# Performance work log

Measured on AMD Instinct MI355X. Metric: run time of the kernel, lower is better.

The kernel has to match this reference:

```python
import jax, jax.numpy as jnp
import numpy as np

PI = 3.1415927410125732
N = 4096
VELOCITY = 5e-7
RC = 3.15e-6          # collision radius
RR = 8e-6             # repulsion radius
RO = 2.5e-5           # orientation radius (Ra = inf -> inside_Ra all-true)
ALPHA = PI            # field of view; < 2*pi so within_view masking is active
DT_TRANS = 1.4e-14    # translational diffusion DT
DR = 0.0028
GAMMA = 25.0
DT = 0.2              # timestep dt
COLLISION_ITERS = 3   # fixed-iteration version of recursive solve_collisions
EPS = 1e-14


def _c(x):  # [N,2] real -> complex64
    return jax.lax.complex(x[..., 0], x[..., 1])


def _r(z):  # complex -> [..., 2] real
    return jnp.stack([z.real, z.imag], axis=-1)


def _anglediff(a, b):
    # torch get_anglediff: wrap angle(a)-angle(b) into (-pi, pi)
    diff = jnp.angle(a) - jnp.angle(b)
    diff = jnp.where(diff <= -PI, jnp.mod(diff, PI), diff)
    return diff - (diff >= PI) * (2.0 * PI)


def _cossim(a, b):
    # nn.CosineSimilarity(dim=1, eps=1e-14) on view_as_real of complex vectors
    dot = a.real * b.real + a.imag * b.imag
    na = jnp.sqrt(a.real ** 2 + a.imag ** 2 + 1e-30)
    nb = jnp.sqrt(b.real ** 2 + b.imag ** 2 + 1e-30)
    return dot / (jnp.maximum(na, EPS) * jnp.maximum(nb, EPS))


def setup_inputs() -> dict:
    key = jax.random.key(0)
    k1, k2, k3, k4, k5 = jax.random.split(key, 5)
    positions = jax.random.normal(k1, (N, 2), jnp.float32) * 5e-4
    ang = jax.random.uniform(k2, (N,), jnp.float32, -PI, PI)
    orientations = jnp.stack([jnp.cos(ang), jnp.sin(ang)], axis=-1)  # unit complex
    Deltas = jax.random.uniform(k3, (1,), jnp.float32, 0.1, 0.6)
    rot_noise = jax.random.normal(k4, (N,), jnp.float32)
    trans_noise = jax.random.normal(k5, (N, 2), jnp.float32)
    return {"positions": positions, "orientations": orientations, "Deltas": Deltas,
            "rot_noise": rot_noise, "trans_noise": trans_noise}


def reference(positions, orientations, Deltas, rot_noise, trans_noise):
    p = _c(positions)      # [N] complex positions
    u = _c(orientations)   # [N] complex orientations
    n = p.shape[0]
    eye = jnp.eye(n, dtype=bool)

    # pairwise direction/distance: dirs[i,j] = p_j - p_i
    dirs = p[None, :] - p[:, None]
    dists = jnp.abs(dirs)

    inside_Rr = (dists <= RR) & ~eye
    inside_Ro = dists <= RO + RC
    # inside_Ra with Ra = inf is all-True

    # angle between separation vector and orientation of the *neighbor* j
    ang_diff = _anglediff(dirs, u[None, :])
    in_front = ang_diff < PI / 2
    within_view = ang_diff < ALPHA  # alpha < 2*pi branch active

    cdtype = p.dtype
    mask_rr = (inside_Rr & in_front).astype(cdtype)
    mask_ra = within_view.astype(cdtype)  # inside_Ra all True
    mask_ro = (inside_Ro & within_view).astype(cdtype)

    n_r = mask_rr.real.sum(axis=1)
    S = (mask_rr @ p) / jnp.maximum(n_r, 1.0) - p * jnp.sign(n_r)
    d = -S

    n_a = mask_ra.real.sum(axis=1)
    cms = (mask_ra @ p) / jnp.maximum(n_a, 1.0)
    Ps = cms - p * jnp.sign(n_a)

    orientation_sums = mask_ro @ u

    leftturns = Ps * jnp.exp(1j * Deltas)
    rightturns = Ps * jnp.exp(-1j * Deltas)

    # T >= T_release branch: pick the turn most aligned with neighbor orientations
    left_closer = _cossim(leftturns, orientation_sums) >= _cossim(rightturns, orientation_sums)
    best_turns = jnp.where(left_closer, leftturns, rightturns)

    d_abs = jnp.abs(d)
    d_safe = jnp.where(d_abs > 0, d, jnp.ones((), cdtype))
    best_safe = jnp.where(jnp.abs(best_turns) > 0, best_turns, jnp.ones((), cdtype))
    angle_to_target = jnp.where(d_abs > 0, _anglediff(d_safe, u), _anglediff(best_safe, u))

    # rotational_noise = randn * sqrt(2*DR); rotation = exp(i*(dt*Gamma*DR*sin + noise*sqrt(dt)))
    rot = jnp.exp(1j * (DT * GAMMA * DR * jnp.sin(angle_to_target)
                        + rot_noise * np.float32(np.sqrt(2 * DR)) * np.float32(np.sqrt(DT))))

    # complex-normal translational noise (per-component std 1/sqrt(2)) * sqrt(2*DT) * sqrt(dt)
    tn = _c(trans_noise) * np.float32(np.sqrt(0.5)) * np.float32(np.sqrt(2 * DT_TRANS))
    translation = DT * VELOCITY * u + tn * np.float32(np.sqrt(DT))

    def collide(i, pos):
        dd = pos[None, :] - pos[:, None]
        dd_nd = jnp.where(eye, jnp.ones((), pos.dtype), dd)  # avoid 0/0 on diagonal
        ab = jnp.where(eye, 0.0, jnp.abs(dd_nd))
        coll = ab <= 2 * RC - jnp.eye(n, dtype=ab.dtype)
        safe = jnp.where(coll, ab, 1.0)
        move = jnp.where(coll, dd / safe * ((2.1 * RC - ab) * 0.5), jnp.zeros((), pos.dtype))
        return pos - move.sum(axis=1)

    new_p = jax.lax.fori_loop(0, COLLISION_ITERS, collide, p + translation)
    new_u = u * rot

    # pack the 5 complex outputs as real [5, N, 2]
    return jnp.stack([_r(new_p), _r(new_u), _r(orientation_sums), _r(leftturns), _r(rightturns)], axis=0)
```

## Files before the change

kernel.cpp:

```cpp
#include <hip/hip_runtime.h>
#include <math.h>

#define NPART 4096
#define NBLK  1024
#define NTHR  256
#define IPB   4
#define SMAX  256
#define PPT   (NPART / NTHR)

constexpr float RORC   = (float)(2.5e-5 + 3.15e-6);
constexpr float RORC2  = RORC * RORC;
constexpr float RRF    = 8e-6f;
constexpr float RR2    = RRF * RRF;
constexpr float TWORC  = (float)(2.0 * 3.15e-6);
constexpr float TWORC2 = TWORC * TWORC;
constexpr float C21RC  = (float)(2.1 * 3.15e-6);
constexpr float RCAND2 = 1.6e-9f;
constexpr float C_ROT  = (float)(0.2 * 25.0 * 0.0028);
constexpr float C_RN1  = (float)0.07483314773547883;
constexpr float C_SQDT = (float)0.4472135954999579;
constexpr float C_TRV  = (float)(0.2 * 5e-7);
constexpr float C_HALF = (float)0.7071067811865476;
constexpr float C_SQ2T = (float)1.6733200530681511e-07;
constexpr float EPSF   = 1e-14f;

__global__ __launch_bounds__(NTHR, 4) void fused_all(
        const float2* __restrict__ pos, const float2* __restrict__ ori,
        const float* __restrict__ Deltas, const float* __restrict__ rot_noise,
        const float2* __restrict__ trans_noise, float2* __restrict__ out) {
    __shared__ float    sred[2 * NTHR];
    __shared__ float    res[5][IPB];
    __shared__ unsigned bmap[NPART / 32];
    __shared__ int      Sidx[SMAX];
    __shared__ float4   posS4[SMAX / 2];
    __shared__ int      scnt;
    float2* posS = (float2*)posS4;
    const float4* __restrict__ pos4 = (const float4*)pos;

    const int tid  = threadIdx.x;
    const int il   = tid >> 6;
    const int lane = tid & 63;
    const int base = blockIdx.x * IPB;
    const int gi   = base + il;

    const float2 pi   = pos[gi];
    const float  delv = Deltas[0];
    float rn_early = 0.f;
    if (tid < IPB) rn_early = rot_noise[base + tid];
    {
        const float2 ow = ori[tid * 16];
        const float2 tw = trans_noise[tid * 16];
        asm volatile("" :: "v"(ow.x), "v"(ow.y), "v"(tw.x), "v"(tw.y));
    }

    if (tid == 0) scnt = IPB;
    if (tid < IPB) Sidx[tid] = base + tid;
    if (tid < NPART / 32) {
        const int seedw = base >> 5;
        bmap[tid] = (tid == seedw) ? (0xFu << (base & 31)) : 0u;
    }

    float mx = 0.f, my = 0.f;
    #pragma unroll
    for (int k = 0; k < PPT; ++k) {
        const float2 v = pos[k * NTHR + tid];
        mx += v.x; my += v.y;
    }
    sred[tid] = mx; sred[NTHR + tid] = my;
    __syncthreads();

    float nr = 0.f, sx = 0.f, sy = 0.f, oxs = 0.f, oys = 0.f;
    #pragma unroll 2
    for (int t = lane; t < NPART / 2; t += 64) {
        const float4 w = pos4[t];
        const float dx0 = w.x - pi.x, dy0 = w.y - pi.y;
        const float r20 = fmaf(dx0, dx0, dy0 * dy0);
        const float dx1 = w.z - pi.x, dy1 = w.w - pi.y;
        const float r21 = fmaf(dx1, dx1, dy1 * dy1);
        if (fminf(r20, r21) > RCAND2) continue;
        if (r20 <= RCAND2) {
            const int j = 2 * t;
            const unsigned bit = 1u << (j & 31);
            const unsigned old = atomicOr(&bmap[j >> 5], bit);
            if (!(old & bit)) {
                const int slot = atomicAdd(&scnt, 1);
                if (slot < SMAX) Sidx[slot] = j;
            }
            if (r20 <= RORC2) {
                const float2 uj = ori[j];
                oxs += uj.x; oys += uj.y;
                if (r20 <= RR2 && r20 > 0.f) {
                    const float dt_ = fmaf(dx0, uj.x, dy0 * uj.y);
                    const float cr_ = fmaf(dy0, uj.x, -dx0 * uj.y);
                    if (!((dt_ <= 0.f) && (cr_ >= 0.f))) {
                        nr += 1.f; sx += w.x; sy += w.y;
                    }
                }
            }
        }
        if (r21 <= RCAND2) {
            const int j = 2 * t + 1;
            const unsigned bit = 1u << (j & 31);
            const unsigned old = atomicOr(&bmap[j >> 5], bit);
            if (!(old & bit)) {
                const int slot = atomicAdd(&scnt, 1);
                if (slot < SMAX) Sidx[slot] = j;
            }
            if (r21 <= RORC2) {
                const float2 uj = ori[j];
                oxs += uj.x; oys += uj.y;
                if (r21 <= RR2 && r21 > 0.f) {
                    const float dt_ = fmaf(dx1, uj.x, dy1 * uj.y);
                    const float cr_ = fmaf(dy1, uj.x, -dx1 * uj.y);
                    if (!((dt_ <= 0.f) && (cr_ >= 0.f))) {
                        nr += 1.f; sx += w.z; sy += w.w;
                    }
                }
            }
        }
    }
    {
        float vals[5] = {nr, sx, sy, oxs, oys};
        #pragma unroll
        for (int q = 0; q < 5; ++q)
            #pragma unroll
            for (int off = 32; off >= 1; off >>= 1)
                vals[q] += __shfl_down(vals[q], off);
        if (lane == 0) {
            res[0][il] = vals[0]; res[1][il] = vals[1]; res[2][il] = vals[2];
            res[3][il] = vals[3]; res[4][il] = vals[4];
        }
    }
    __syncthreads();

    const int nS = (scnt < SMAX) ? scnt : SMAX;
    if (tid < 128) {
        sred[tid]        += sred[tid + 128];
        sred[NTHR + tid] += sred[NTHR + tid + 128];
    }
    if (tid < nS) {
        const int p = Sidx[tid];
        const float2 pq = pos[p];
        const float2 uu = ori[p];
        const float2 tn = trans_noise[p];
        posS[tid] = make_float2(
            pq.x + (C_TRV * uu.x + ((tn.x * C_HALF) * C_SQ2T) * C_SQDT),
            pq.y + (C_TRV * uu.y + ((tn.y * C_HALF) * C_SQ2T) * C_SQDT));
    }
    __syncthreads();

    if (tid < 64) {
        sred[tid]        += sred[tid + 64];
        sred[NTHR + tid] += sred[NTHR + tid + 64];
    }
    __syncthreads();

    float cmx = 0.f, cmy = 0.f;
    if (il == 0) {
        float vx = sred[lane];
        float vy = sred[NTHR + lane];
        #pragma unroll
        for (int off = 32; off >= 1; off >>= 1) {
            vx += __shfl_down(vx, off);
            vy += __shfl_down(vy, off);
        }
        cmx = __shfl(vx, 0) * (1.f / NPART);
        cmy = __shfl(vy, 0) * (1.f / NPART);
    }

    if (tid < IPB) {
        const int g2 = base + tid;
        const float2 p = pos[g2];
        const float2 u = ori[g2];
        const float nrv = res[0][tid], sxv = res[1][tid], syv = res[2][tid];
        const float osx = res[3][tid], osy = res[4][tid];

        const float inv = 1.f / fmaxf(nrv, 1.f);
        const float sg  = (nrv > 0.f) ? 1.f : 0.f;
        const float Sx = sxv * inv - p.x * sg;
        const float Sy = syv * inv - p.y * sg;
        const float dxv = -Sx, dyv = -Sy;

        const float Psx = cmx - p.x;
        const float Psy = cmy - p.y;

        float sd, cd;
        sincosf(delv, &sd, &cd);
        const float Lx = Psx * cd - Psy * sd;
        const float Ly = Psx * sd + Psy * cd;
        const float Rx = Psx * cd + Psy * sd;
        const float Ry = Psy * cd - Psx * sd;

        const float no  = fmaxf(sqrtf(osx * osx + osy * osy + 1e-30f), EPSF);
        const float nl  = fmaxf(sqrtf(Lx * Lx + Ly * Ly + 1e-30f), EPSF);
        const float nrr = fmaxf(sqrtf(Rx * Rx + Ry * Ry + 1e-30f), EPSF);
        const float csl = (Lx * osx + Ly * osy) / (nl * no);
        const float csr = (Rx * osx + Ry * osy) / (nrr * no);
        const bool left = (csl >= csr);
        const float bx = left ? Lx : Rx;
        const float by = left ? Ly : Ry;

        float cx, cy;
        if (dxv != 0.f || dyv != 0.f)    { cx = dxv; cy = dyv; }
        else if (bx != 0.f || by != 0.f) { cx = bx;  cy = by;  }
        else                             { cx = 1.f; cy = 0.f; }

        const float dt_ = cx * u.x + cy * u.y;
        const float cr_ = cy * u.x - cx * u.y;
        const float sin_t = cr_ / sqrtf(dt_ * dt_ + cr_ * cr_);

        const float ang = C_ROT * sin_t + (rn_early * C_RN1) * C_SQDT;
        float sa, ca;
        sincosf(ang, &sa, &ca);
        out[1 * NPART + g2] = make_float2(u.x * ca - u.y * sa,
                                          u.x * sa + u.y * ca);
        out[2 * NPART + g2] = make_float2(osx, osy);
        out[3 * NPART + g2] = make_float2(Lx, Ly);
        out[4 * NPART + g2] = make_float2(Rx, Ry);
    }

    for (int pass = 0; pass < 3; ++pass) {
        float px = 1e9f, py = 1e9f, ax = 0.f, ay = 0.f;
        const bool mv = (tid < nS);
        if (mv) { px = posS[tid].x; py = posS[tid].y; }
        int b = 0;
        for (; b + 4 <= nS; b += 4) {
            const float4 w0 = posS4[(b >> 1)];
            const float4 w1 = posS4[(b >> 1) + 1];
            const float bxs[4] = {w0.x, w0.z, w1.x, w1.z};
            const float bys[4] = {w0.y, w0.w, w1.y, w1.w};
            #pragma unroll
            for (int s = 0; s < 4; ++s) {
                const float dx = bxs[s] - px, dy = bys[s] - py;
                const float r2 = fmaf(dx, dx, dy * dy);
                if (r2 <= TWORC2 && r2 > 0.f) {
                    const float ab = sqrtf(r2);
                    const float sc = (C21RC - ab) * 0.5f / ab;
                    ax = fmaf(dx, sc, ax);
                    ay = fmaf(dy, sc, ay);
                }
            }
        }
        for (; b < nS; ++b) {
            const float2 pb = posS[b];
            const float dx = pb.x - px, dy = pb.y - py;
            const float r2 = fmaf(dx, dx, dy * dy);
            if (r2 <= TWORC2 && r2 > 0.f) {
                const float ab = sqrtf(r2);
                const float sc = (C21RC - ab) * 0.5f / ab;
                ax = fmaf(dx, sc, ax);
                ay = fmaf(dy, sc, ay);
            }
        }
        __syncthreads();
        if (mv) posS[tid] = make_float2(px - ax, py - ay);
        __syncthreads();
    }
    if (tid < IPB)
        out[0 * NPART + base + tid] = posS[tid];
}

extern "C" void kernel_launch(void* const* d_in, const int* in_sizes, int n_in,
                              void* d_out, int out_size, void* d_ws, size_t ws_size,
                              hipStream_t stream) {
    const float2* pos = (const float2*)d_in[0];
    const float2* ori = (const float2*)d_in[1];
    const float*  del = (const float*)d_in[2];
    const float*  rn  = (const float*)d_in[3];
    const float2* tn  = (const float2*)d_in[4];
    float2* o2 = (float2*)d_out;
    (void)d_ws; (void)ws_size;

    fused_all<<<dim3(NBLK), dim3(NTHR), 0, stream>>>(pos, ori, del, rn, tn, o2);
}
```

Before: 85.00 us.

## Split each particle's neighbor scan across two wavefronts with 512-thread blocks

Doubles the block size so that two wavefronts, rather than one, scan the pairwise neighbour range for each of the four particles per block, each covering half of the positions. The per-wave partial sums are stored in shared memory and combined before the final per-particle math, and the centre-of-mass reduction gains an extra level. This shortens the serial scan each wave performs, in exchange for larger blocks, more reduction work and an extra shared-memory combine. Occupancy may change because of the new launch bounds.

Result: no change. 86.03 us (+1.2%).

```diff
diff --git a/kernel.cpp b/kernel.cpp
--- a/kernel.cpp
+++ b/kernel.cpp
@@ -3,10 +3,11 @@
 
 #define NPART 4096
 #define NBLK  1024
-#define NTHR  256
+#define NTHR  512
 #define IPB   4
 #define SMAX  256
 #define PPT   (NPART / NTHR)
+#define HALF4 (NPART / 2 / 2)
 
 constexpr float RORC   = (float)(2.5e-5 + 3.15e-6);
 constexpr float RORC2  = RORC * RORC;
@@ -24,12 +25,12 @@
 constexpr float C_SQ2T = (float)1.6733200530681511e-07;
 constexpr float EPSF   = 1e-14f;
 
-__global__ __launch_bounds__(NTHR, 4) void fused_all(
+__global__ __launch_bounds__(NTHR, 8) void fused_all(
         const float2* __restrict__ pos, const float2* __restrict__ ori,
         const float* __restrict__ Deltas, const float* __restrict__ rot_noise,
         const float2* __restrict__ trans_noise, float2* __restrict__ out) {
     __shared__ float    sred[2 * NTHR];
-    __shared__ float    res[5][IPB];
+    __shared__ float    resW[5][8];
     __shared__ unsigned bmap[NPART / 32];
     __shared__ int      Sidx[SMAX];
     __shared__ float4   posS4[SMAX / 2];
@@ -38,7 +39,9 @@
     const float4* __restrict__ pos4 = (const float4*)pos;
 
     const int tid  = threadIdx.x;
-    const int il   = tid >> 6;
+    const int w    = tid >> 6;
+    const int il   = w >> 1;
+    const int h    = w & 1;
     const int lane = tid & 63;
     const int base = blockIdx.x * IPB;
     const int gi   = base + il;
@@ -48,8 +51,8 @@
     float rn_early = 0.f;
     if (tid < IPB) rn_early = rot_noise[base + tid];
     {
-        const float2 ow = ori[tid * 16];
-        const float2 tw = trans_noise[tid * 16];
+        const float2 ow = ori[tid * 8];
+        const float2 tw = trans_noise[tid * 8];
         asm volatile("" :: "v"(ow.x), "v"(ow.y), "v"(tw.x), "v"(tw.y));
     }
 
@@ -71,11 +74,11 @@
 
     float nr = 0.f, sx = 0.f, sy = 0.f, oxs = 0.f, oys = 0.f;
     #pragma unroll 2
-    for (int t = lane; t < NPART / 2; t += 64) {
-        const float4 w = pos4[t];
-        const float dx0 = w.x - pi.x, dy0 = w.y - pi.y;
+    for (int t = h * HALF4 + lane; t < (h + 1) * HALF4; t += 64) {
+        const float4 wv = pos4[t];
+        const float dx0 = wv.x - pi.x, dy0 = wv.y - pi.y;
         const float r20 = fmaf(dx0, dx0, dy0 * dy0);
-        const float dx1 = w.z - pi.x, dy1 = w.w - pi.y;
+        const float dx1 = wv.z - pi.x, dy1 = wv.w - pi.y;
         const float r21 = fmaf(dx1, dx1, dy1 * dy1);
         if (fminf(r20, r21) > RCAND2) continue;
         if (r20 <= RCAND2) {
@@ -93,7 +96,7 @@
                     const float dt_ = fmaf(dx0, uj.x, dy0 * uj.y);
                     const float cr_ = fmaf(dy0, uj.x, -dx0 * uj.y);
                     if (!((dt_ <= 0.f) && (cr_ >= 0.f))) {
-                        nr += 1.f; sx += w.x; sy += w.y;
+                        nr += 1.f; sx += wv.x; sy += wv.y;
                     }
                 }
             }
@@ -113,7 +116,7 @@
                     const float dt_ = fmaf(dx1, uj.x, dy1 * uj.y);
                     const float cr_ = fmaf(dy1, uj.x, -dx1 * uj.y);
                     if (!((dt_ <= 0.f) && (cr_ >= 0.f))) {
-                        nr += 1.f; sx += w.z; sy += w.w;
+                        nr += 1.f; sx += wv.z; sy += wv.w;
                     }
                 }
             }
@@ -127,16 +130,16 @@
             for (int off = 32; off >= 1; off >>= 1)
                 vals[q] += __shfl_down(vals[q], off);
         if (lane == 0) {
-            res[0][il] = vals[0]; res[1][il] = vals[1]; res[2][il] = vals[2];
-            res[3][il] = vals[3]; res[4][il] = vals[4];
+            resW[0][w] = vals[0]; resW[1][w] = vals[1]; resW[2][w] = vals[2];
+            resW[3][w] = vals[3]; resW[4][w] = vals[4];
         }
     }
     __syncthreads();
 
     const int nS = (scnt < SMAX) ? scnt : SMAX;
-    if (tid < 128) {
-        sred[tid]        += sred[tid + 128];
-        sred[NTHR + tid] += sred[NTHR + tid + 128];
+    if (tid < 256) {
+        sred[tid]        += sred[tid + 256];
+        sred[NTHR + tid] += sred[NTHR + tid + 256];
     }
     if (tid < nS) {
         const int p = Sidx[tid];
@@ -149,16 +152,16 @@
     }
     __syncthreads();
 
-    if (tid < 64) {
-        sred[tid]        += sred[tid + 64];
-        sred[NTHR + tid] += sred[NTHR + tid + 64];
+    if (tid < 128) {
+        sred[tid]        += sred[tid + 128];
+        sred[NTHR + tid] += sred[NTHR + tid + 128];
     }
     __syncthreads();
 
     float cmx = 0.f, cmy = 0.f;
-    if (il == 0) {
-        float vx = sred[lane];
-        float vy = sred[NTHR + lane];
+    if (w == 0) {
+        float vx = sred[lane]        + sred[lane + 64];
+        float vy = sred[NTHR + lane] + sred[NTHR + lane + 64];
         #pragma unroll
         for (int off = 32; off >= 1; off >>= 1) {
             vx += __shfl_down(vx, off);
@@ -172,8 +175,12 @@
         const int g2 = base + tid;
         const float2 p = pos[g2];
         const float2 u = ori[g2];
-        const float nrv = res[0][tid], sxv = res[1][tid], syv = res[2][tid];
-        const float osx = res[3][tid], osy = res[4][tid];
+        const int wa = 2 * tid, wb = 2 * tid + 1;
+        const float nrv = resW[0][wa] + resW[0][wb];
+        const float sxv = resW[1][wa] + resW[1][wb];
+        const float syv = resW[2][wa] + resW[2][wb];
+        const float osx = resW[3][wa] + resW[3][wb];
+        const float osy = resW[4][wa] + resW[4][wb];
 
         const float inv = 1.f / fmaxf(nrv, 1.f);
         const float sg  = (nrv > 0.f) ? 1.f : 0.f;
```
